# Performance work log

Hardware: AMD Instinct MI355X
Metric: run time of the kernel (lower is better)

Reference implementation:

```python
import jax, jax.numpy as jnp
import numpy as np

ALPHA = 0.2   # LeakyReLU slope
EPS = 1e-5    # BatchNorm eps
NEG = -1e9


def setup_inputs() -> dict:
    key = jax.random.key(0)
    ks = jax.random.split(key, 12)
    B, N, F_IN, O, H, L = 1024, 100, 65, 32, 4, 5
    D = O * H  # 128 hidden per node
    X = jax.random.normal(ks[0], (B, N, F_IN), dtype=jnp.float32)
    A = jax.random.randint(ks[1], (B, N, N), 0, 2).astype(jnp.float32)
    s = lambda fan: 1.0 / np.sqrt(fan)
    # layer 0 heads (input dim 65), layers 1..4 heads (input dim 128)
    W0 = jax.random.normal(ks[2], (H, F_IN, O), dtype=jnp.float32) * s(F_IN)
    a0 = jax.random.normal(ks[3], (H, 2 * O), dtype=jnp.float32) * s(2 * O)
    Wl = jax.random.normal(ks[4], (L - 1, H, D, O), dtype=jnp.float32) * s(D)
    al = jax.random.normal(ks[5], (L - 1, H, 2 * O), dtype=jnp.float32) * s(2 * O)
    # proj: Linear(12800,1024) BN ReLU Linear(1024,128) BN ReLU
    pW1 = jax.random.normal(ks[6], (D * N, 1024), dtype=jnp.float32) * s(D * N)
    pb1 = jnp.zeros((1024,), jnp.float32)
    g1 = jnp.ones((1024,), jnp.float32)
    be1 = jnp.zeros((1024,), jnp.float32)
    pW2 = jax.random.normal(ks[7], (1024, 128), dtype=jnp.float32) * s(1024)
    pb2 = jnp.zeros((128,), jnp.float32)
    g2 = jnp.ones((128,), jnp.float32)
    be2 = jnp.zeros((128,), jnp.float32)
    return dict(X=X, A=A, W0=W0, a0=a0, Wl=Wl, al=al,
                pW1=pW1, pb1=pb1, g1=g1, be1=be1,
                pW2=pW2, pb2=pb2, g2=g2, be2=be2)


def _gat(x, A, W, a):
    # x:(B,N,F) W:(H,F,O) a:(H,2O) -> (B,N,H*O); batched multi-head GAT
    O = W.shape[-1]
    h = jnp.einsum('bnf,hfo->bhno', x, W)                  # (B,H,N,O)
    e_src = jnp.einsum('bhno,ho->bhn', h, a[:, :O])
    e_dst = jnp.einsum('bhno,ho->bhn', h, a[:, O:])
    e = jax.nn.leaky_relu(e_src[:, :, :, None] + e_dst[:, :, None, :], ALPHA)
    e = jnp.where(A[:, None, :, :] > 0, e, NEG)            # adjacency mask
    att = jax.nn.softmax(e, axis=-1)                       # (B,H,N,N)
    out = jax.nn.elu(jnp.einsum('bhnm,bhmo->bhno', att, h))
    B, _, N, _ = out.shape
    return out.transpose(0, 2, 1, 3).reshape(B, N, -1)     # concat heads


def _bn(x, g, b):
    # eval-mode BatchNorm1d with running_mean=0, running_var=1
    return g * x / jnp.sqrt(1.0 + EPS) + b


def reference(X, A, W0, a0, Wl, al, pW1, pb1, g1, be1, pW2, pb2, g2, be2):
    x = _gat(X, A, W0, a0)
    for i in range(Wl.shape[0]):
        x = _gat(x, A, Wl[i], al[i])
    B = X.shape[0]
    out = x.reshape(B, -1)
    out = jax.nn.relu(_bn(out @ pW1 + pb1, g1, be1))
    out = jax.nn.relu(_bn(out @ pW2 + pb2, g2, be2))
    return out
```

## Files before the change

### kernel.cpp

```cpp
#include <hip/hip_runtime.h>
#include <math.h>

typedef __attribute__((ext_vector_type(8))) short short8;
typedef __attribute__((ext_vector_type(4))) float f32x4;
typedef __attribute__((ext_vector_type(4))) uint  uint4v;

constexpr int Bb = 1024, Nn = 100, Hh = 4, Oo = 32, Dd = 128;
constexpr int K1 = 12800, N1 = 1024, M1 = 1024, SK = 8;

__device__ __forceinline__ ushort f2bf(float f) {
    uint u = __float_as_uint(f);
    return (ushort)((u + 0x7FFFu + ((u >> 16) & 1u)) >> 16);
}
__device__ __forceinline__ float bf2f(ushort h) {
    return __uint_as_float(((uint)h) << 16);
}
__device__ __forceinline__ short8 mk8(uint a, uint b, uint c, uint d) {
    uint4v v = {a, b, c, d};
    return __builtin_bit_cast(short8, v);
}
__device__ __forceinline__ int swzb(int row, int kb)  { return row * 256 + (kb ^ ((row & 7) << 4)); }

#define OFF_HTH 0
#define OFF_HTL 8192
#define OFF_WTH 16384
#define OFF_WTL 24576
#define OFF_AB  32768
#define OFF_ASV 34560
#define OFF_ESV 34816
#define OFF_EDV 35328
#define OFF_INV 35840
#define GAT_LDS 36352

__global__ __launch_bounds__(256) void pack_A(const float* __restrict__ A, uint* __restrict__ AW)
{
    const int b = blockIdx.x;
    const float4* Ab = (const float4*)(A + (size_t)b * 10000);
    for (int t = threadIdx.x; t < 400; t += 256) {
        const int row = t >> 2, word = t & 3;
        uint bits = 0;
        if (word < 3) {
            #pragma unroll
            for (int j = 0; j < 8; ++j) {
                float4 v = Ab[row * 25 + word * 8 + j];
                uint b4 = (v.x > 0.f ? 1u : 0u) | (v.y > 0.f ? 2u : 0u)
                        | (v.z > 0.f ? 4u : 0u) | (v.w > 0.f ? 8u : 0u);
                bits |= b4 << (j * 4);
            }
        } else {
            float4 v = Ab[row * 25 + 24];
            bits = (v.x > 0.f ? 1u : 0u) | (v.y > 0.f ? 2u : 0u)
                 | (v.z > 0.f ? 4u : 0u) | (v.w > 0.f ? 8u : 0u);
        }
        AW[(size_t)b * 400 + t] = bits;
    }
}

template<int F, int KD>
__global__ __launch_bounds__(512, 4) void gat_fused(
    const float* __restrict__ xin,
    const uint*  __restrict__ AW,
    const float* __restrict__ W,
    const float* __restrict__ av,
    float* __restrict__ xout)
{
    extern __shared__ char smem[];
    char*  HTH = smem + OFF_HTH;
    char*  HTL = smem + OFF_HTL;
    char*  WTH = smem + OFF_WTH;
    char*  WTL = smem + OFF_WTL;
    uint*  ABu = (uint*)(smem + OFF_AB);
    float* ASV = (float*)(smem + OFF_ASV);
    float* ESV = (float*)(smem + OFF_ESV);
    float* EDV = (float*)(smem + OFF_EDV);
    float* INV = (float*)(smem + OFF_INV);

    const int tid = threadIdx.x;
    const int task = (blockIdx.x & 7) * 512 + (blockIdx.x >> 3);
    const int b = task >> 2, hd = task & 3;
    const int w = tid >> 6, lane = tid & 63;
    const int c16 = lane & 15, r16 = lane >> 4;

    const float* xg = xin + (size_t)b * Nn * F;

    if (F == 65) {
        uint4 z = make_uint4(0, 0, 0, 0);
        #pragma unroll
        for (int i = 0; i < 2; ++i)
            *(uint4*)(smem + OFF_WTH + (i * 512 + tid) * 16) = z;
        __syncthreads();
    }

    const int nA = (w * 16 + c16 < 100) ? (w * 16 + c16) : 99;
    float4 xpre[8];
    if (F == 128 && w < 7) {
        #pragma unroll
        for (int d = 0; d < 4; ++d) {
            const float* px = xg + (size_t)nA * 128 + d * 32 + r16 * 8;
            xpre[2 * d]     = *(const float4*)(px);
            xpre[2 * d + 1] = *(const float4*)(px + 4);
        }
    }

    {
        const float4* Wg4 = (const float4*)(W + (size_t)hd * F * 32);
        #pragma unroll
        for (int it = 0; it < 2; ++it) {
            int id = it * 512 + tid;
            if (id < F * 8) {
                int f = id >> 3, o4 = (id & 7) * 4;
                float4 v = Wg4[id];
                ushort h0 = f2bf(v.x), l0 = f2bf(v.x - bf2f(h0));
                ushort h1 = f2bf(v.y), l1 = f2bf(v.y - bf2f(h1));
                ushort h2 = f2bf(v.z), l2 = f2bf(v.z - bf2f(h2));
                ushort h3 = f2bf(v.w), l3 = f2bf(v.w - bf2f(h3));
                *(ushort*)(WTH + swzb(o4 + 0, 2 * f)) = h0; *(ushort*)(WTL + swzb(o4 + 0, 2 * f)) = l0;
                *(ushort*)(WTH + swzb(o4 + 1, 2 * f)) = h1; *(ushort*)(WTL + swzb(o4 + 1, 2 * f)) = l1;
                *(ushort*)(WTH + swzb(o4 + 2, 2 * f)) = h2; *(ushort*)(WTL + swzb(o4 + 2, 2 * f)) = l2;
                *(ushort*)(WTH + swzb(o4 + 3, 2 * f)) = h3; *(ushort*)(WTL + swzb(o4 + 3, 2 * f)) = l3;
            }
        }
    }
    if (tid < 64) ASV[tid] = av[hd * 64 + tid];
    {
        const int idA = tid - 64;
        if (idA >= 0 && idA < 400) ABu[idA] = AW[(size_t)b * 400 + idA];
        else if (idA >= 400 && idA < 448) ABu[idA] = 0u;
    }
    if (tid < 256) {
        char* base = (tid & 128) ? HTL : HTH;
        const int rr = (tid >> 2) & 31, sl = 12 + (tid & 3);
        *(uint4*)(base + swzb(rr, sl * 16)) = make_uint4(0, 0, 0, 0);
    }
    if (tid < 28) { ESV[100 + tid] = 0.f; EDV[100 + tid] = 0.f; }
    __syncthreads();

    if (w < 7) {
        f32x4 acc0 = {0.f, 0.f, 0.f, 0.f}, acc1 = {0.f, 0.f, 0.f, 0.f};
        #pragma unroll
        for (int d = 0; d < KD; ++d) {
            float xv[8];
            if (F == 128) {
                float4 v0 = xpre[2 * d], v1 = xpre[2 * d + 1];
                xv[0] = v0.x; xv[1] = v0.y; xv[2] = v0.z; xv[3] = v0.w;
                xv[4] = v1.x; xv[5] = v1.y; xv[6] = v1.z; xv[7] = v1.w;
            } else {
                const int f0 = d * 32 + r16 * 8;
                #pragma unroll
                for (int j = 0; j < 8; ++j) {
                    int f = f0 + j;
                    xv[j] = (f < 65) ? xg[(size_t)nA * 65 + f] : 0.f;
                }
            }
            uint hu[4], lu[4];
            #pragma unroll
            for (int i = 0; i < 4; ++i) {
                uint u0 = __float_as_uint(xv[2 * i]);
                uint u1 = __float_as_uint(xv[2 * i + 1]);
                float l0 = xv[2 * i]     - __uint_as_float(u0 & 0xFFFF0000u);
                float l1 = xv[2 * i + 1] - __uint_as_float(u1 & 0xFFFF0000u);
                hu[i] = __builtin_amdgcn_perm(u1, u0, 0x07060302u);
                lu[i] = __builtin_amdgcn_perm(__float_as_uint(l1), __float_as_uint(l0), 0x07060302u);
            }
            short8 ah = mk8(hu[0], hu[1], hu[2], hu[3]);
            short8 al = mk8(lu[0], lu[1], lu[2], lu[3]);
            const int kb = d * 64 + r16 * 16;
            short8 bh0 = *(const short8*)(WTH + swzb(c16, kb));
            short8 bl0 = *(const short8*)(WTL + swzb(c16, kb));
            short8 bh1 = *(const short8*)(WTH + swzb(16 + c16, kb));
            short8 bl1 = *(const short8*)(WTL + swzb(16 + c16, kb));
            acc0 = __builtin_amdgcn_mfma_f32_16x16x32_bf16(ah, bh0, acc0, 0, 0, 0);
            acc0 = __builtin_amdgcn_mfma_f32_16x16x32_bf16(al, bh0, acc0, 0, 0, 0);
            acc0 = __builtin_amdgcn_mfma_f32_16x16x32_bf16(ah, bl0, acc0, 0, 0, 0);
            acc1 = __builtin_amdgcn_mfma_f32_16x16x32_bf16(ah, bh1, acc1, 0, 0, 0);
            acc1 = __builtin_amdgcn_mfma_f32_16x16x32_bf16(al, bh1, acc1, 0, 0, 0);
            acc1 = __builtin_amdgcn_mfma_f32_16x16x32_bf16(ah, bl1, acc1, 0, 0, 0);
        }
        const int n0 = w * 16 + r16 * 4;
        if (n0 < 100) {
            ushort h0 = f2bf(acc0[0]), l0 = f2bf(acc0[0] - bf2f(h0));
            ushort h1 = f2bf(acc0[1]), l1 = f2bf(acc0[1] - bf2f(h1));
            ushort h2 = f2bf(acc0[2]), l2 = f2bf(acc0[2] - bf2f(h2));
            ushort h3 = f2bf(acc0[3]), l3 = f2bf(acc0[3] - bf2f(h3));
            uint2 uh; uh.x = (uint)h0 | ((uint)h1 << 16); uh.y = (uint)h2 | ((uint)h3 << 16);
            uint2 ul; ul.x = (uint)l0 | ((uint)l1 << 16); ul.y = (uint)l2 | ((uint)l3 << 16);
            *(uint2*)(HTH + swzb(c16, 2 * n0)) = uh;
            *(uint2*)(HTL + swzb(c16, 2 * n0)) = ul;
            h0 = f2bf(acc1[0]); l0 = f2bf(acc1[0] - bf2f(h0));
            h1 = f2bf(acc1[1]); l1 = f2bf(acc1[1] - bf2f(h1));
            h2 = f2bf(acc1[2]); l2 = f2bf(acc1[2] - bf2f(h2));
            h3 = f2bf(acc1[3]); l3 = f2bf(acc1[3] - bf2f(h3));
            uh.x = (uint)h0 | ((uint)h1 << 16); uh.y = (uint)h2 | ((uint)h3 << 16);
            ul.x = (uint)l0 | ((uint)l1 << 16); ul.y = (uint)l2 | ((uint)l3 << 16);
            *(uint2*)(HTH + swzb(16 + c16, 2 * n0)) = uh;
            *(uint2*)(HTL + swzb(16 + c16, 2 * n0)) = ul;
        }
        const float as0 = ASV[c16], as1 = ASV[16 + c16];
        const float ad0 = ASV[32 + c16], ad1 = ASV[48 + c16];
        #pragma unroll
        for (int r = 0; r < 4; ++r) {
            float vs = acc0[r] * as0 + acc1[r] * as1;
            float vd = acc0[r] * ad0 + acc1[r] * ad1;
            #pragma unroll
            for (int mk = 1; mk <= 8; mk <<= 1) {
                vs += __shfl_xor(vs, mk, 64);
                vd += __shfl_xor(vd, mk, 64);
            }
            if (c16 == 0 && n0 + r < 100) { ESV[n0 + r] = vs; EDV[n0 + r] = vd; }
        }
    }
    __syncthreads();

    f32x4 acc0 = {0.f, 0.f, 0.f, 0.f}, acc1 = {0.f, 0.f, 0.f, 0.f};
    if (w < 7) {
        const int np = w * 16 + c16;
        const float esn = ESV[np];
        const uint4 abv = *(const uint4*)(ABu + np * 4);
        float rowsum = 0.f;
        #pragma unroll
        for (int d = 0; d < 4; ++d) {
            const uint wrd = (d == 0) ? abv.x : (d == 1) ? abv.y : (d == 2) ? abv.z : abv.w;
            const float4 ea = *(const float4*)(EDV + d * 32 + r16 * 8);
            const float4 eb = *(const float4*)(EDV + d * 32 + r16 * 8 + 4);
            float p0, p1, p2, p3, p4, p5, p6, p7, e;
            e = esn + ea.x; e = e > 0.f ? e : 0.2f * e; p0 = ((wrd >> (r16 * 8 + 0)) & 1u) ? __expf(e) : 0.f;
            e = esn + ea.y; e = e > 0.f ? e : 0.2f * e; p1 = ((wrd >> (r16 * 8 + 1)) & 1u) ? __expf(e) : 0.f;
            e = esn + ea.z; e = e > 0.f ? e : 0.2f * e; p2 = ((wrd >> (r16 * 8 + 2)) & 1u) ? __expf(e) : 0.f;
            e = esn + ea.w; e = e > 0.f ? e : 0.2f * e; p3 = ((wrd >> (r16 * 8 + 3)) & 1u) ? __expf(e) : 0.f;
            e = esn + eb.x; e = e > 0.f ? e : 0.2f * e; p4 = ((wrd >> (r16 * 8 + 4)) & 1u) ? __expf(e) : 0.f;
            e = esn + eb.y; e = e > 0.f ? e : 0.2f * e; p5 = ((wrd >> (r16 * 8 + 5)) & 1u) ? __expf(e) : 0.f;
            e = esn + eb.z; e = e > 0.f ? e : 0.2f * e; p6 = ((wrd >> (r16 * 8 + 6)) & 1u) ? __expf(e) : 0.f;
            e = esn + eb.w; e = e > 0.f ? e : 0.2f * e; p7 = ((wrd >> (r16 * 8 + 7)) & 1u) ? __expf(e) : 0.f;
            rowsum += p0 + p1 + p2 + p3 + p4 + p5 + p6 + p7;
            ushort h0 = f2bf(p0), h1 = f2bf(p1), h2 = f2bf(p2), h3 = f2bf(p3);
            ushort h4 = f2bf(p4), h5 = f2bf(p5), h6 = f2bf(p6), h7 = f2bf(p7);
            ushort q0 = f2bf(p0 - bf2f(h0)), q1 = f2bf(p1 - bf2f(h1));
            ushort q2 = f2bf(p2 - bf2f(h2)), q3 = f2bf(p3 - bf2f(h3));
            ushort q4 = f2bf(p4 - bf2f(h4)), q5 = f2bf(p5 - bf2f(h5));
            ushort q6 = f2bf(p6 - bf2f(h6)), q7 = f2bf(p7 - bf2f(h7));
            short8 ph = mk8((uint)h0 | ((uint)h1 << 16), (uint)h2 | ((uint)h3 << 16),
                            (uint)h4 | ((uint)h5 << 16), (uint)h6 | ((uint)h7 << 16));
            short8 pl = mk8((uint)q0 | ((uint)q1 << 16), (uint)q2 | ((uint)q3 << 16),
                            (uint)q4 | ((uint)q5 << 16), (uint)q6 | ((uint)q7 << 16));
            const int kb = d * 64 + r16 * 16;
            short8 bh0 = *(const short8*)(HTH + swzb(c16, kb));
            short8 bl0 = *(const short8*)(HTL + swzb(c16, kb));
            short8 bh1 = *(const short8*)(HTH + swzb(16 + c16, kb));
            short8 bl1 = *(const short8*)(HTL + swzb(16 + c16, kb));
            acc0 = __builtin_amdgcn_mfma_f32_16x16x32_bf16(ph, bh0, acc0, 0, 0, 0);
            acc0 = __builtin_amdgcn_mfma_f32_16x16x32_bf16(ph, bl0, acc0, 0, 0, 0);
            acc0 = __builtin_amdgcn_mfma_f32_16x16x32_bf16(pl, bh0, acc0, 0, 0, 0);
            acc1 = __builtin_amdgcn_mfma_f32_16x16x32_bf16(ph, bh1, acc1, 0, 0, 0);
            acc1 = __builtin_amdgcn_mfma_f32_16x16x32_bf16(ph, bl1, acc1, 0, 0, 0);
            acc1 = __builtin_amdgcn_mfma_f32_16x16x32_bf16(pl, bh1, acc1, 0, 0, 0);
        }
        rowsum += __shfl_xor(rowsum, 16, 64);
        rowsum += __shfl_xor(rowsum, 32, 64);
        if (r16 == 0 && np < 100) INV[np] = 1.0f / rowsum;
    }
    __syncthreads();

    if (w < 7) {
        const int n0 = w * 16 + r16 * 4;
        float* xo = xout + (size_t)b * Nn * Dd + hd * 32;
        #pragma unroll
        for (int r = 0; r < 4; ++r) {
            const int n = n0 + r;
            if (n < 100) {
                const float inv = INV[n];
                float v0 = acc0[r] * inv; v0 = v0 > 0.f ? v0 : expm1f(v0);
                float v1 = acc1[r] * inv; v1 = v1 > 0.f ? v1 : expm1f(v1);
                xo[(size_t)n * Dd + c16] = v0;
                xo[(size_t)n * Dd + 16 + c16] = v1;
            }
        }
    }
}

#define G1_LDS 73728
__device__ __forceinline__ int aofs(int r, int kb) { return r * 144 + kb; }
__device__ __forceinline__ int bofs(int n, int kb) { return n * 144 + (kb ^ (((n >> 3) & 1) << 4)); }

__global__ __launch_bounds__(512, 4) void gemm1_mfma(
    const float* __restrict__ Ag, const float* __restrict__ Bg,
    float* __restrict__ part)
{
    extern __shared__ char sm[];
    char* AH = sm;
    char* AL = sm + 18432;
    char* BH = sm + 36864;
    char* BL = sm + 55296;

    const int tid = threadIdx.x;
    const int pb = blockIdx.x;
    const int task = (pb & 7) * 64 + (pb >> 3);
    const int mb = task & 7, g = task >> 3;
    const int nb = g & 7, z = g >> 3;
    const int m0 = mb * 128, n0 = nb * 128;
    const int k0 = z * 1600;

    const int w = tid >> 6, lane = tid & 63;
    const int wn = w & 3, wm = w >> 2;
    const int c16 = lane & 15, r16 = lane >> 4;

    const int ra = tid >> 2, kq = tid & 3;
    const int bn = tid >> 2, kq4 = tid & 3;

    const float* Aptr = Ag + (size_t)(m0 + ra) * K1 + k0 + kq * 16;
    const float* Bptr = Bg + (size_t)(k0 + kq4 * 16) * N1 + n0 + bn;

    f32x4 acc[4][2];
    #pragma unroll
    for (int i = 0; i < 4; ++i)
        #pragma unroll
        for (int j = 0; j < 2; ++j) acc[i][j] = (f32x4){0.f, 0.f, 0.f, 0.f};

    float a_reg[16];
    float b_reg[16];
    #pragma unroll
    for (int q = 0; q < 4; ++q) *(float4*)&a_reg[q * 4] = *(const float4*)(Aptr + q * 4);
    #pragma unroll
    for (int j = 0; j < 16; ++j) b_reg[j] = Bptr[(size_t)j * N1];

    for (int it = 0; it < 25; ++it) {
        __syncthreads();
        {
            uint hi[8], lo[8];
            #pragma unroll
            for (int i = 0; i < 8; ++i) {
                uint u0 = __float_as_uint(a_reg[2 * i]);
                uint u1 = __float_as_uint(a_reg[2 * i + 1]);
                float l0 = a_reg[2 * i]     - __uint_as_float(u0 & 0xFFFF0000u);
                float l1 = a_reg[2 * i + 1] - __uint_as_float(u1 & 0xFFFF0000u);
                hi[i] = __builtin_amdgcn_perm(u1, u0, 0x07060302u);
                lo[i] = __builtin_amdgcn_perm(__float_as_uint(l1), __float_as_uint(l0), 0x07060302u);
            }
            const int ab = aofs(ra, kq * 32);
            *(uint4*)(AH + ab)      = make_uint4(hi[0], hi[1], hi[2], hi[3]);
            *(uint4*)(AH + ab + 16) = make_uint4(hi[4], hi[5], hi[6], hi[7]);
            *(uint4*)(AL + ab)      = make_uint4(lo[0], lo[1], lo[2], lo[3]);
            *(uint4*)(AL + ab + 16) = make_uint4(lo[4], lo[5], lo[6], lo[7]);
        }
        {
            uint hi[8], lo[8];
            #pragma unroll
            for (int i = 0; i < 8; ++i) {
                uint u0 = __float_as_uint(b_reg[2 * i]);
                uint u1 = __float_as_uint(b_reg[2 * i + 1]);
                float l0 = b_reg[2 * i]     - __uint_as_float(u0 & 0xFFFF0000u);
                float l1 = b_reg[2 * i + 1] - __uint_as_float(u1 & 0xFFFF0000u);
                hi[i] = __builtin_amdgcn_perm(u1, u0, 0x07060302u);
                lo[i] = __builtin_amdgcn_perm(__float_as_uint(l1), __float_as_uint(l0), 0x07060302u);
            }
            const int bb0 = bofs(bn, kq4 * 32);
            const int bb1 = bofs(bn, kq4 * 32 + 16);
            *(uint4*)(BH + bb0) = make_uint4(hi[0], hi[1], hi[2], hi[3]);
            *(uint4*)(BH + bb1) = make_uint4(hi[4], hi[5], hi[6], hi[7]);
            *(uint4*)(BL + bb0) = make_uint4(lo[0], lo[1], lo[2], lo[3]);
            *(uint4*)(BL + bb1) = make_uint4(lo[4], lo[5], lo[6], lo[7]);
        }
        __syncthreads();

        if (it < 24) {
            Aptr += 64;
            Bptr += (size_t)64 * N1;
            #pragma unroll
            for (int q = 0; q < 4; ++q) *(float4*)&a_reg[q * 4] = *(const float4*)(Aptr + q * 4);
            #pragma unroll
            for (int j = 0; j < 16; ++j) b_reg[j] = Bptr[(size_t)j * N1];
        }

        #pragma unroll
        for (int ks = 0; ks < 2; ++ks) {
            const int kb = ks * 64 + r16 * 16;
            short8 bh[2], bl[2];
            #pragma unroll
            for (int nf = 0; nf < 2; ++nf) {
                const int nr = wn * 32 + nf * 16 + c16;
                bh[nf] = *(const short8*)(BH + bofs(nr, kb));
                bl[nf] = *(const short8*)(BL + bofs(nr, kb));
            }
            #pragma unroll
            for (int mf = 0; mf < 4; ++mf) {
                const int ar = wm * 64 + mf * 16 + c16;
                short8 ah = *(const short8*)(AH + aofs(ar, kb));
                short8 al = *(const short8*)(AL + aofs(ar, kb));
                #pragma unroll
                for (int nf = 0; nf < 2; ++nf) {
                    acc[mf][nf] = __builtin_amdgcn_mfma_f32_16x16x32_bf16(ah, bh[nf], acc[mf][nf], 0, 0, 0);
                    acc[mf][nf] = __builtin_amdgcn_mfma_f32_16x16x32_bf16(al, bh[nf], acc[mf][nf], 0, 0, 0);
                    acc[mf][nf] = __builtin_amdgcn_mfma_f32_16x16x32_bf16(ah, bl[nf], acc[mf][nf], 0, 0, 0);
                }
            }
        }
    }

    float* pz = part + (size_t)z * M1 * N1;
    #pragma unroll
    for (int mf = 0; mf < 4; ++mf) {
        const int m = m0 + wm * 64 + mf * 16 + r16 * 4;
        #pragma unroll
        for (int nf = 0; nf < 2; ++nf) {
            const int n = n0 + wn * 32 + nf * 16 + c16;
            #pragma unroll
            for (int r = 0; r < 4; ++r)
                pz[(size_t)(m + r) * N1 + n] = acc[mf][nf][r];
        }
    }
}

__global__ __launch_bounds__(256) void bn1_reduce(
    const float* __restrict__ part, const float* __restrict__ pb1,
    const float* __restrict__ g1, const float* __restrict__ be1,
    float* __restrict__ y1)
{
    const int idx = blockIdx.x * 256 + threadIdx.x;
    float s = 0.f;
    #pragma unroll
    for (int z = 0; z < SK; ++z) s += part[(size_t)z * M1 * N1 + idx];
    const int j = idx & (N1 - 1);
    s += pb1[j];
    const float rbn = 1.0f / sqrtf(1.0f + 1e-5f);
    s = g1[j] * s * rbn + be1[j];
    y1[idx] = fmaxf(s, 0.f);
}

__global__ __launch_bounds__(128) void gemm2_bn(
    const float* __restrict__ y1, const float* __restrict__ W2,
    const float* __restrict__ pb2, const float* __restrict__ g2,
    const float* __restrict__ be2, float* __restrict__ out)
{
    __shared__ __align__(16) float xr[1024];
    const int tid = threadIdx.x, m = blockIdx.x;
    for (int i = tid; i < 1024; i += 128) xr[i] = y1[(size_t)m * 1024 + i];
    __syncthreads();
    float acc = 0.f;
    #pragma unroll 8
    for (int k = 0; k < 1024; ++k) acc += xr[k] * W2[k * 128 + tid];
    acc += pb2[tid];
    const float rbn = 1.0f / sqrtf(1.0f + 1e-5f);
    acc = g2[tid] * acc * rbn + be2[tid];
    out[(size_t)m * 128 + tid] = fmaxf(acc, 0.f);
}

extern "C" void kernel_launch(void* const* d_in, const int* in_sizes, int n_in,
                              void* d_out, int out_size, void* d_ws, size_t ws_size,
                              hipStream_t stream)
{
    const float* X   = (const float*)d_in[0];
    const float* A   = (const float*)d_in[1];
    const float* W0  = (const float*)d_in[2];
    const float* a0  = (const float*)d_in[3];
    const float* Wl  = (const float*)d_in[4];
    const float* al  = (const float*)d_in[5];
    const float* pW1 = (const float*)d_in[6];
    const float* pb1 = (const float*)d_in[7];
    const float* g1  = (const float*)d_in[8];
    const float* be1 = (const float*)d_in[9];
    const float* pW2 = (const float*)d_in[10];
    const float* pb2 = (const float*)d_in[11];
    const float* g2  = (const float*)d_in[12];
    const float* be2 = (const float*)d_in[13];
    float* out = (float*)d_out;

    float* ws = (float*)d_ws;
    float* xa = ws;
    float* xb = xa + (size_t)Bb * Nn * Dd;
    float* y1 = xb + (size_t)Bb * Nn * Dd;
    float* part = xb;
    uint*  AW = (uint*)y1;

    (void)hipFuncSetAttribute(reinterpret_cast<const void*>(gat_fused<65, 3>),
                              hipFuncAttributeMaxDynamicSharedMemorySize, GAT_LDS);
    (void)hipFuncSetAttribute(reinterpret_cast<const void*>(gat_fused<128, 4>),
                              hipFuncAttributeMaxDynamicSharedMemorySize, GAT_LDS);
    (void)hipFuncSetAttribute(reinterpret_cast<const void*>(gemm1_mfma),
                              hipFuncAttributeMaxDynamicSharedMemorySize, G1_LDS);

    pack_A<<<dim3(Bb), 256, 0, stream>>>(A, AW);
    gat_fused<65, 3><<<dim3(Bb * Hh), 512, GAT_LDS, stream>>>(X, AW, W0, a0, xa);
    const float* src = xa; float* dst = xb;
    for (int l = 1; l < 5; ++l) {
        gat_fused<128, 4><<<dim3(Bb * Hh), 512, GAT_LDS, stream>>>(
            src, AW, Wl + (size_t)(l - 1) * Hh * Dd * Oo, al + (size_t)(l - 1) * Hh * 2 * Oo, dst);
        float* t = (float*)src; src = dst; dst = t;
    }
    gemm1_mfma<<<dim3(512), 512, G1_LDS, stream>>>(src, pW1, part);
    bn1_reduce<<<dim3((M1 * N1) / 256), 256, 0, stream>>>(part, pb1, g1, be1, y1);
    gemm2_bn<<<dim3(M1), 128, 0, stream>>>(y1, pW2, pb2, g2, be2, out);
}
```

Baseline: 477.3 us.

## Store GAT activations pre-split as bf16 hi/lo and double-buffer gemm1 prefetch

GAT layers now write their ELU outputs as separate bf16 high and low-residual arrays instead of fp32. Later GAT layers and the projection GEMM load those split operands directly, which removes the per-element split arithmetic from their inner loops while keeping the total bytes moved the same. gemm1 also prefetches two K-steps ahead with double-buffered registers, aiming to hide global load latency better. The costs are higher register pressure under a 128-VGPR launch bound and narrower 2-byte scattered stores in the GAT epilogue.

```diff
diff --git a/kernel.cpp b/kernel.cpp
--- a/kernel.cpp
+++ b/kernel.cpp
@@ -18,6 +18,10 @@
 __device__ __forceinline__ short8 mk8(uint a, uint b, uint c, uint d) {
     uint4v v = {a, b, c, d};
     return __builtin_bit_cast(short8, v);
+}
+__device__ __forceinline__ short8 u4s8(uint4 v) {
+    uint4v t = {v.x, v.y, v.z, v.w};
+    return __builtin_bit_cast(short8, t);
 }
 __device__ __forceinline__ int swzb(int row, int kb)  { return row * 256 + (kb ^ ((row & 7) << 4)); }
 
@@ -58,11 +62,14 @@
 
 template<int F, int KD>
 __global__ __launch_bounds__(512, 4) void gat_fused(
-    const float* __restrict__ xin,
-    const uint*  __restrict__ AW,
-    const float* __restrict__ W,
-    const float* __restrict__ av,
-    float* __restrict__ xout)
+    const float*  __restrict__ xinF,
+    const ushort* __restrict__ xinH,
+    const ushort* __restrict__ xinL,
+    const uint*   __restrict__ AW,
+    const float*  __restrict__ W,
+    const float*  __restrict__ av,
+    ushort* __restrict__ outH,
+    ushort* __restrict__ outL)
 {
     extern __shared__ char smem[];
     char*  HTH = smem + OFF_HTH;
@@ -81,8 +88,6 @@
     const int w = tid >> 6, lane = tid & 63;
     const int c16 = lane & 15, r16 = lane >> 4;
 
-    const float* xg = xin + (size_t)b * Nn * F;
-
     if (F == 65) {
         uint4 z = make_uint4(0, 0, 0, 0);
         #pragma unroll
@@ -92,13 +97,14 @@
     }
 
     const int nA = (w * 16 + c16 < 100) ? (w * 16 + c16) : 99;
-    float4 xpre[8];
+    uint4 xph[4], xpl[4];
     if (F == 128 && w < 7) {
+        const ushort* xh = xinH + (size_t)b * 12800 + (size_t)nA * 128 + r16 * 8;
+        const ushort* xl = xinL + (size_t)b * 12800 + (size_t)nA * 128 + r16 * 8;
         #pragma unroll
         for (int d = 0; d < 4; ++d) {
-            const float* px = xg + (size_t)nA * 128 + d * 32 + r16 * 8;
-            xpre[2 * d]     = *(const float4*)(px);
-            xpre[2 * d + 1] = *(const float4*)(px + 4);
+            xph[d] = *(const uint4*)(xh + d * 32);
+            xpl[d] = *(const uint4*)(xl + d * 32);
         }
     }
 
@@ -139,31 +145,32 @@
         f32x4 acc0 = {0.f, 0.f, 0.f, 0.f}, acc1 = {0.f, 0.f, 0.f, 0.f};
         #pragma unroll
         for (int d = 0; d < KD; ++d) {
-            float xv[8];
+            short8 ah, al;
             if (F == 128) {
-                float4 v0 = xpre[2 * d], v1 = xpre[2 * d + 1];
-                xv[0] = v0.x; xv[1] = v0.y; xv[2] = v0.z; xv[3] = v0.w;
-                xv[4] = v1.x; xv[5] = v1.y; xv[6] = v1.z; xv[7] = v1.w;
+                ah = u4s8(xph[d]);
+                al = u4s8(xpl[d]);
             } else {
+                const float* xg = xinF + (size_t)b * Nn * 65;
                 const int f0 = d * 32 + r16 * 8;
+                float xv[8];
                 #pragma unroll
                 for (int j = 0; j < 8; ++j) {
                     int f = f0 + j;
                     xv[j] = (f < 65) ? xg[(size_t)nA * 65 + f] : 0.f;
                 }
-            }
-            uint hu[4], lu[4];
-            #pragma unroll
-            for (int i = 0; i < 4; ++i) {
-                uint u0 = __float_as_uint(xv[2 * i]);
-                uint u1 = __float_as_uint(xv[2 * i + 1]);
-                float l0 = xv[2 * i]     - __uint_as_float(u0 & 0xFFFF0000u);
-                float l1 = xv[2 * i + 1] - __uint_as_float(u1 & 0xFFFF0000u);
-                hu[i] = __builtin_amdgcn_perm(u1, u0, 0x07060302u);
-                lu[i] = __builtin_amdgcn_perm(__float_as_uint(l1), __float_as_uint(l0), 0x07060302u);
-            }
-            short8 ah = mk8(hu[0], hu[1], hu[2], hu[3]);
-            short8 al = mk8(lu[0], lu[1], lu[2], lu[3]);
+                uint hu[4], lu[4];
+                #pragma unroll
+                for (int i = 0; i < 4; ++i) {
+                    uint u0 = __float_as_uint(xv[2 * i]);
+                    uint u1 = __float_as_uint(xv[2 * i + 1]);
+                    float l0 = xv[2 * i]     - __uint_as_float(u0 & 0xFFFF0000u);
+                    float l1 = xv[2 * i + 1] - __uint_as_float(u1 & 0xFFFF0000u);
+                    hu[i] = __builtin_amdgcn_perm(u1, u0, 0x07060302u);
+                    lu[i] = __builtin_amdgcn_perm(__float_as_uint(l1), __float_as_uint(l0), 0x07060302u);
+                }
+                ah = mk8(hu[0], hu[1], hu[2], hu[3]);
+                al = mk8(lu[0], lu[1], lu[2], lu[3]);
+            }
             const int kb = d * 64 + r16 * 16;
             short8 bh0 = *(const short8*)(WTH + swzb(c16, kb));
             short8 bl0 = *(const short8*)(WTL + swzb(c16, kb));
@@ -262,7 +269,7 @@
 
     if (w < 7) {
         const int n0 = w * 16 + r16 * 4;
-        float* xo = xout + (size_t)b * Nn * Dd + hd * 32;
+        const size_t obase = (size_t)b * 12800 + hd * 32;
         #pragma unroll
         for (int r = 0; r < 4; ++r) {
             const int n = n0 + r;
@@ -270,8 +277,12 @@
                 const float inv = INV[n];
                 float v0 = acc0[r] * inv; v0 = v0 > 0.f ? v0 : expm1f(v0);
                 float v1 = acc1[r] * inv; v1 = v1 > 0.f ? v1 : expm1f(v1);
-                xo[(size_t)n * Dd + c16] = v0;
-                xo[(size_t)n * Dd + 16 + c16] = v1;
+                ushort h0 = f2bf(v0), l0 = f2bf(v0 - bf2f(h0));
+                ushort h1 = f2bf(v1), l1 = f2bf(v1 - bf2f(h1));
+                outH[obase + n * 128 + c16] = h0;
+                outL[obase + n * 128 + c16] = l0;
+                outH[obase + n * 128 + 16 + c16] = h1;
+                outL[obase + n * 128 + 16 + c16] = l1;
             }
         }
     }
@@ -282,8 +293,8 @@
 __device__ __forceinline__ int bofs(int n, int kb) { return n * 144 + (kb ^ (((n >> 3) & 1) << 4)); }
 
 __global__ __launch_bounds__(512, 4) void gemm1_mfma(
-    const float* __restrict__ Ag, const float* __restrict__ Bg,
-    float* __restrict__ part)
+    const ushort* __restrict__ AHg, const ushort* __restrict__ ALg,
+    const float* __restrict__ Bg, float* __restrict__ part)
 {
     extern __shared__ char sm[];
     char* AH = sm;
@@ -306,8 +317,9 @@
     const int ra = tid >> 2, kq = tid & 3;
     const int bn = tid >> 2, kq4 = tid & 3;
 
-    const float* Aptr = Ag + (size_t)(m0 + ra) * K1 + k0 + kq * 16;
-    const float* Bptr = Bg + (size_t)(k0 + kq4 * 16) * N1 + n0 + bn;
+    const ushort* Ah0 = AHg + (size_t)(m0 + ra) * K1 + k0 + kq * 16;
+    const ushort* Al0 = ALg + (size_t)(m0 + ra) * K1 + k0 + kq * 16;
+    const float*  Bb0 = Bg + ((size_t)k0 + kq4 * 16) * N1 + n0 + bn;
 
     f32x4 acc[4][2];
     #pragma unroll
@@ -315,40 +327,37 @@
         #pragma unroll
         for (int j = 0; j < 2; ++j) acc[i][j] = (f32x4){0.f, 0.f, 0.f, 0.f};
 
-    float a_reg[16];
-    float b_reg[16];
+    uint4 aH[2][2], aL[2][2];
+    float bR[2][16];
     #pragma unroll
-    for (int q = 0; q < 4; ++q) *(float4*)&a_reg[q * 4] = *(const float4*)(Aptr + q * 4);
-    #pragma unroll
-    for (int j = 0; j < 16; ++j) b_reg[j] = Bptr[(size_t)j * N1];
+    for (int pf = 0; pf < 2; ++pf) {
+        const int off = pf * 64;
+        aH[pf][0] = *(const uint4*)(Ah0 + off);
+        aH[pf][1] = *(const uint4*)(Ah0 + off + 8);
+        aL[pf][0] = *(const uint4*)(Al0 + off);
+        aL[pf][1] = *(const uint4*)(Al0 + off + 8);
+        #pragma unroll
+        for (int j = 0; j < 16; ++j) bR[pf][j] = Bb0[(size_t)(off + j) * N1];
+    }
 
     for (int it = 0; it < 25; ++it) {
+        const int cur = it & 1;
         __syncthreads();
         {
-            uint hi[8], lo[8];
-            #pragma unroll
-            for (int i = 0; i < 8; ++i) {
-                uint u0 = __float_as_uint(a_reg[2 * i]);
-                uint u1 = __float_as_uint(a_reg[2 * i + 1]);
-                float l0 = a_reg[2 * i]     - __uint_as_float(u0 & 0xFFFF0000u);
-                float l1 = a_reg[2 * i + 1] - __uint_as_float(u1 & 0xFFFF0000u);
-                hi[i] = __builtin_amdgcn_perm(u1, u0, 0x07060302u);
-                lo[i] = __builtin_amdgcn_perm(__float_as_uint(l1), __float_as_uint(l0), 0x07060302u);
-            }
             const int ab = aofs(ra, kq * 32);
-            *(uint4*)(AH + ab)      = make_uint4(hi[0], hi[1], hi[2], hi[3]);
-            *(uint4*)(AH + ab + 16) = make_uint4(hi[4], hi[5], hi[6], hi[7]);
-            *(uint4*)(AL + ab)      = make_uint4(lo[0], lo[1], lo[2], lo[3]);
-            *(uint4*)(AL + ab + 16) = make_uint4(lo[4], lo[5], lo[6], lo[7]);
+            *(uint4*)(AH + ab)      = aH[cur][0];
+            *(uint4*)(AH + ab + 16) = aH[cur][1];
+            *(uint4*)(AL + ab)      = aL[cur][0];
+            *(uint4*)(AL + ab + 16) = aL[cur][1];
         }
         {
             uint hi[8], lo[8];
             #pragma unroll
             for (int i = 0; i < 8; ++i) {
-                uint u0 = __float_as_uint(b_reg[2 * i]);
-                uint u1 = __float_as_uint(b_reg[2 * i + 1]);
-                float l0 = b_reg[2 * i]     - __uint_as_float(u0 & 0xFFFF0000u);
-                float l1 = b_reg[2 * i + 1] - __uint_as_float(u1 & 0xFFFF0000u);
+                uint u0 = __float_as_uint(bR[cur][2 * i]);
+                uint u1 = __float_as_uint(bR[cur][2 * i + 1]);
+                float l0 = bR[cur][2 * i]     - __uint_as_float(u0 & 0xFFFF0000u);
+                float l1 = bR[cur][2 * i + 1] - __uint_as_float(u1 & 0xFFFF0000u);
                 hi[i] = __builtin_amdgcn_perm(u1, u0, 0x07060302u);
                 lo[i] = __builtin_amdgcn_perm(__float_as_uint(l1), __float_as_uint(l0), 0x07060302u);
             }
@@ -361,13 +370,14 @@
         }
         __syncthreads();
 
-        if (it < 24) {
-            Aptr += 64;
-            Bptr += (size_t)64 * N1;
-            #pragma unroll
-            for (int q = 0; q < 4; ++q) *(float4*)&a_reg[q * 4] = *(const float4*)(Aptr + q * 4);
-            #pragma unroll
-            for (int j = 0; j < 16; ++j) b_reg[j] = Bptr[(size_t)j * N1];
+        if (it < 23) {
+            const int off = (it + 2) * 64;
+            aH[cur][0] = *(const uint4*)(Ah0 + off);
+            aH[cur][1] = *(const uint4*)(Ah0 + off + 8);
+            aL[cur][0] = *(const uint4*)(Al0 + off);
+            aL[cur][1] = *(const uint4*)(Al0 + off + 8);
+            #pragma unroll
+            for (int j = 0; j < 16; ++j) bR[cur][j] = Bb0[(size_t)(off + j) * N1];
         }
 
         #pragma unroll
@@ -469,6 +479,8 @@
     float* y1 = xb + (size_t)Bb * Nn * Dd;
     float* part = xb;
     uint*  AW = (uint*)y1;
+    ushort* xaH = (ushort*)xa; ushort* xaL = xaH + (size_t)Bb * 12800;
+    ushort* xbH = (ushort*)xb; ushort* xbL = xbH + (size_t)Bb * 12800;
 
     (void)hipFuncSetAttribute(reinterpret_cast<const void*>(gat_fused<65, 3>),
                               hipFuncAttributeMaxDynamicSharedMemorySize, GAT_LDS);
@@ -478,14 +490,19 @@
                               hipFuncAttributeMaxDynamicSharedMemorySize, G1_LDS);
 
     pack_A<<<dim3(Bb), 256, 0, stream>>>(A, AW);
-    gat_fused<65, 3><<<dim3(Bb * Hh), 512, GAT_LDS, stream>>>(X, AW, W0, a0, xa);
-    const float* src = xa; float* dst = xb;
+    gat_fused<65, 3><<<dim3(Bb * Hh), 512, GAT_LDS, stream>>>(
+        X, nullptr, nullptr, AW, W0, a0, xaH, xaL);
+    const ushort *sH = xaH, *sL = xaL;
+    ushort *dH = xbH, *dL = xbL;
     for (int l = 1; l < 5; ++l) {
         gat_fused<128, 4><<<dim3(Bb * Hh), 512, GAT_LDS, stream>>>(
-            src, AW, Wl + (size_t)(l - 1) * Hh * Dd * Oo, al + (size_t)(l - 1) * Hh * 2 * Oo, dst);
-        float* t = (float*)src; src = dst; dst = t;
-    }
-    gemm1_mfma<<<dim3(512), 512, G1_LDS, stream>>>(src, pW1, part);
+            nullptr, sH, sL, AW,
+            Wl + (size_t)(l - 1) * Hh * Dd * Oo, al + (size_t)(l - 1) * Hh * 2 * Oo, dH, dL);
+        ushort* t;
+        t = (ushort*)sH; sH = dH; dH = t;
+        t = (ushort*)sL; sL = dL; dL = t;
+    }
+    gemm1_mfma<<<dim3(512), 512, G1_LDS, stream>>>(xaH, xaL, pW1, part);
     bn1_reduce<<<dim3((M1 * N1) / 256), 256, 0, stream>>>(part, pb1, g1, be1, y1);
     gemm2_bn<<<dim3(M1), 128, 0, stream>>>(y1, pW2, pb2, g2, be2, out);
 }
```

Result: slower. 674.6 us (+41.3%).
